# Kernel tuning notes

Measured on AMD Instinct MI355X. Metric: run time of the kernel, lower is better.

## Reference

```python
import jax, jax.numpy as jnp
import numpy as np

B, S, D, H = 2, 2048, 1024, 16
DK = D // H

def setup_inputs() -> dict:
    key = jax.random.key(0)
    ks = jax.random.split(key, 12)
    scale = 1.0 / np.sqrt(D)
    return {
        "q": jax.random.normal(ks[0], (B, S, D), jnp.float32),
        "k": jax.random.normal(ks[1], (B, S, D), jnp.float32),
        "v": jax.random.normal(ks[2], (B, S, D), jnp.float32),
        "mask": jax.random.randint(ks[3], (B, 1, S, S), 0, 2, jnp.int32),
        "w_q": jax.random.normal(ks[4], (D, D), jnp.float32) * scale,
        "b_q": jnp.zeros((D,), jnp.float32),
        "w_k": jax.random.normal(ks[5], (D, D), jnp.float32) * scale,
        "b_k": jnp.zeros((D,), jnp.float32),
        "w_v": jax.random.normal(ks[6], (D, D), jnp.float32) * scale,
        "b_v": jnp.zeros((D,), jnp.float32),
        "w_o": jax.random.normal(ks[7], (D, D), jnp.float32) * scale,
        "b_o": jnp.zeros((D,), jnp.float32),
    }

def reference(q, k, v, mask, w_q, b_q, w_k, b_k, w_v, b_v, w_o, b_o):
    # projections (nn.Linear: x @ W^T + b)
    Q = q @ w_q.T + b_q  # [B,S,D]
    K = k @ w_k.T + b_k
    V = v @ w_v.T + b_v
    # split heads -> [B,H,S,DK]
    Q = Q.reshape(B, S, H, DK).transpose(0, 2, 1, 3)
    K = K.reshape(B, S, H, DK).transpose(0, 2, 1, 3)
    V = V.reshape(B, S, H, DK).transpose(0, 2, 1, 3)
    scores = jnp.einsum("bhqd,bhkd->bhqk", Q, K) / jnp.sqrt(jnp.float32(DK))
    scores = jnp.where(mask == 0, jnp.float32(-1e9), scores)
    attn = jax.nn.softmax(scores, axis=-1)  # dropout p=0 -> identity
    x = jnp.einsum("bhqk,bhkd->bhqd", attn, V)
    x = x.transpose(0, 2, 1, 3).reshape(B, S, D)
    return x @ w_o.T + b_o
```

## Files before the change

### kernel.cpp

```cpp
#include <hip/hip_runtime.h>
#include <hip/hip_bf16.h>
#include <cstdint>
#include <cstddef>

typedef short bf16x8 __attribute__((ext_vector_type(8)));
typedef short bf16x4v __attribute__((ext_vector_type(4)));
typedef float f32x4 __attribute__((ext_vector_type(4)));
typedef __hip_bfloat16 bf16;

constexpr int Bb = 2, Ss = 2048, Dd = 1024, Hh = 16, DKk = 64;

__device__ __forceinline__ void async_lds16(void* lds, const void* g) {
  __builtin_amdgcn_global_load_lds(
      (const __attribute__((address_space(1))) void*)g,
      (__attribute__((address_space(3))) void*)lds, 16, 0, 0);
}

__device__ __forceinline__ float bf2f(bf16 x) { return __bfloat162float(x); }
__device__ __forceinline__ short f2bf(float x) {
  bf16 h = __float2bfloat16(x);
  return *(short*)&h;
}
__device__ __forceinline__ short f2bf_fast(float x) {
  return (short)((__float_as_uint(x) + 0x8000u) >> 16);
}
__device__ __forceinline__ uint32_t pack2bf(float a, float b) {
  return ((__float_as_uint(a) + 0x8000u) >> 16) |
         ((__float_as_uint(b) + 0x8000u) & 0xffff0000u);
}
__device__ __forceinline__ float bfs2f(short s) {
  return __uint_as_float(((uint32_t)(uint16_t)s) << 16);
}

struct CvtArgs {
  const float* src[12];
  short* dst[12];
  int n[12];
  int count;
};

__global__ __launch_bounds__(256)
void cvt_all(CvtArgs a)
{
  const int t = blockIdx.y;
  if (t >= a.count) return;
  const float* s = a.src[t];
  short* d = a.dst[t];
  const int n = a.n[t];
  const int stride = gridDim.x * blockDim.x * 4;
  for (int i = (blockIdx.x * blockDim.x + threadIdx.x) * 4; i < n; i += stride) {
    const float4 v = *(const float4*)(s + i);
    bf16x4v o;
    o[0] = f2bf(v.x); o[1] = f2bf(v.y); o[2] = f2bf(v.z); o[3] = f2bf(v.w);
    *(bf16x4v*)(d + i) = o;
  }
}

__global__ __launch_bounds__(256)
void pack_mask(const int* __restrict__ mask, uint32_t* __restrict__ bits)
{
  const int i = blockIdx.x * 256 + threadIdx.x;
  const unsigned long long bal = __ballot(mask[i] != 0);
  if ((threadIdx.x & 63) == 0)
    *(unsigned long long*)(bits + (i >> 5)) = bal;
}

__global__ __launch_bounds__(256, 3)
void gemm_bt(const bf16* __restrict__ A0, const bf16* __restrict__ A1, const bf16* __restrict__ A2,
             const bf16* __restrict__ W0, const bf16* __restrict__ W1, const bf16* __restrict__ W2,
             const bf16* __restrict__ b0, const bf16* __restrict__ b1, const bf16* __restrict__ b2,
             void* __restrict__ O0, void* __restrict__ O1, void* __restrict__ O2,
             float scale0, int wf32, int vtrans)
{
  extern __shared__ char smem[];
  const int mt  = blockIdx.x;
  const int by  = blockIdx.y;
  const int mat = by >> 3;
  const int nt  = by & 7;
  const bf16* A    = (mat == 0) ? A0 : (mat == 1) ? A1 : A2;
  const bf16* W    = (mat == 0) ? W0 : (mat == 1) ? W1 : W2;
  const bf16* bias = (mat == 0) ? b0 : (mat == 1) ? b1 : b2;
  void*       Out  = (mat == 0) ? O0 : (mat == 1) ? O1 : O2;
  const float scale = (mat == 0) ? scale0 : 1.0f;

  const int tid  = threadIdx.x;
  const int w    = tid >> 6;
  const int lane = tid & 63;
  const int quad = lane >> 4;
  const int l16  = lane & 15;
  const int wm   = (w & 1) * 64;
  const int wn   = (w >> 1) * 64;

  const int srow = lane >> 3;
  const int sseg = (lane & 7) ^ srow;

  const char* Abytes = (const char*)A;
  const char* Wbytes = (const char*)W;

  f32x4 acc[4][4];
#pragma unroll
  for (int i = 0; i < 4; ++i)
#pragma unroll
    for (int j = 0; j < 4; ++j) acc[i][j] = f32x4{0.f, 0.f, 0.f, 0.f};

  for (int kt = 0; kt < 16; ++kt) {
    __syncthreads();
#pragma unroll
    for (int c = 0; c < 4; ++c) {
      const int r0 = w * 32 + c * 8;
      async_lds16(smem + r0 * 128,
                  Abytes + (size_t)(mt * 128 + r0 + srow) * 2048 + kt * 128 + sseg * 16);
      async_lds16(smem + 16384 + r0 * 128,
                  Wbytes + (size_t)(nt * 128 + r0 + srow) * 2048 + kt * 128 + sseg * 16);
    }
    __syncthreads();
#pragma unroll
    for (int s = 0; s < 2; ++s) {
      bf16x8 af[4], bfg[4];
#pragma unroll
      for (int mb = 0; mb < 4; ++mb) {
        const int row = wm + mb * 16 + l16;
        af[mb] = *(const bf16x8*)(smem + row * 128 + (((4 * s + quad) ^ (row & 7)) * 16));
      }
#pragma unroll
      for (int nb = 0; nb < 4; ++nb) {
        const int row = wn + nb * 16 + l16;
        bfg[nb] = *(const bf16x8*)(smem + 16384 + row * 128 + (((4 * s + quad) ^ (row & 7)) * 16));
      }
#pragma unroll
      for (int mb = 0; mb < 4; ++mb)
#pragma unroll
        for (int nb = 0; nb < 4; ++nb)
          acc[mb][nb] = __builtin_amdgcn_mfma_f32_16x16x32_bf16(af[mb], bfg[nb], acc[mb][nb], 0, 0, 0);
    }
  }

  if (vtrans && mat == 2) {
    __syncthreads();
#pragma unroll
    for (int nb = 0; nb < 4; ++nb) {
      const int dk = wn + nb * 16 + l16;
      const float bv = bf2f(bias[nt * 128 + dk]);
#pragma unroll
      for (int mb = 0; mb < 4; ++mb) {
        const int s0 = wm + mb * 16 + quad * 4;
        bf16x4v pk;
#pragma unroll
        for (int r = 0; r < 4; ++r) pk[r] = f2bf_fast(acc[mb][nb][r] + bv);
        *(bf16x4v*)(smem + dk * 256 + (((s0 >> 3) ^ (dk & 15)) * 16) + (s0 & 7) * 2) = pk;
      }
    }
    __syncthreads();
    const int bidx  = (mt * 128) >> 11;
    const int sbase = (mt * 128) & 2047;
#pragma unroll
    for (int i = 0; i < 8; ++i) {
      const int dk  = i * 16 + (tid >> 4);
      const int seg = tid & 15;
      bf16x8 vrow = *(const bf16x8*)(smem + dk * 256 + ((seg ^ (dk & 15)) * 16));
      *(bf16x8*)((bf16*)Out + (size_t)bidx * 2097152 + (size_t)(nt * 128 + dk) * 2048
                 + sbase + seg * 8) = vrow;
    }
  } else {
#pragma unroll
    for (int nb = 0; nb < 4; ++nb) {
      const int col = nt * 128 + wn + nb * 16 + l16;
      const float bv = bf2f(bias[col]);
#pragma unroll
      for (int mb = 0; mb < 4; ++mb) {
#pragma unroll
        for (int r = 0; r < 4; ++r) {
          const int row = mt * 128 + wm + mb * 16 + quad * 4 + r;
          const float val = (acc[mb][nb][r] + bv) * scale;
          const size_t idx = (size_t)row * 1024 + col;
          if (wf32) ((float*)Out)[idx] = val;
          else      ((bf16*)Out)[idx] = *(bf16*)&(short&)*(short[]){f2bf_fast(val)};
        }
      }
    }
  }
}

__global__ __launch_bounds__(256, 3)
void attn(const bf16* __restrict__ Qp, const bf16* __restrict__ Kp,
          const bf16* __restrict__ VpT, const uint32_t* __restrict__ mbits,
          bf16* __restrict__ Opart, float* __restrict__ Lpart)
{
  __shared__ char smem[49152];
  char* Kb = smem;
  char* Vt = smem + 16384;
  char* Ph = smem + 32768;

  const int tile  = blockIdx.x;
  const int split = blockIdx.y;
  const int qt = tile & 15, h = (tile >> 4) & 15, b = tile >> 8;
  const int tid = threadIdx.x, w = tid >> 6, lane = tid & 63;
  const int quad = lane >> 4, l16 = lane & 15;
  const int qb = qt * 128;
  const size_t headoff = (size_t)b * (Ss * Dd) + h * DKk;

  const int kc0 = (split == 0) ? 0 : (split == 1) ? 6 : 11;
  const int kc1 = (split == 0) ? 6 : (split == 1) ? 11 : 16;

  bf16x8 qf[2][2];
#pragma unroll
  for (int set = 0; set < 2; ++set)
#pragma unroll
    for (int s2 = 0; s2 < 2; ++s2) {
      const int row = qb + w * 32 + set * 16 + l16;
      qf[set][s2] = *(const bf16x8*)(Qp + headoff + (size_t)row * Dd + s2 * 32 + quad * 8);
    }

  f32x4 o[2][4];
  float Lacc[2] = {0.f, 0.f};
#pragma unroll
  for (int set = 0; set < 2; ++set)
#pragma unroll
    for (int nbk = 0; nbk < 4; ++nbk) o[set][nbk] = f32x4{0.f, 0.f, 0.f, 0.f};

  const uint32_t* mrow0 = mbits + (size_t)(b * Ss + qb + w * 32 + l16) * 64;
  const uint32_t* mrow1 = mrow0 + 16 * 64;

  char* Preg = (w < 2) ? smem : Ph;
  const int prowbase = (w & 1) * 32;

  for (int kc = kc0; kc < kc1; ++kc) {
    const int kb = kc * 128;
    __syncthreads();
#pragma unroll
    for (int c = 0; c < 4; ++c) {
      {
        const int row = c * 32 + w * 8 + (lane >> 3);
        const int seg = (lane & 7) ^ (row & 7);
        async_lds16(Kb + c * 4096 + w * 1024,
                    Kp + headoff + (size_t)(kb + row) * Dd + seg * 8);
      }
      {
        const int row = c * 16 + w * 4 + (lane >> 4);
        const int seg = (lane & 15) ^ (row & 15);
        async_lds16(Vt + c * 4096 + w * 1024,
                    VpT + (size_t)b * 2097152 + (size_t)(h * 64 + row) * 2048 + kb + seg * 8);
      }
    }
    __syncthreads();

    f32x4 sc[2][8];
#pragma unroll
    for (int set = 0; set < 2; ++set)
#pragma unroll
      for (int nb = 0; nb < 8; ++nb) sc[set][nb] = f32x4{0.f, 0.f, 0.f, 0.f};
#pragma unroll
    for (int s2 = 0; s2 < 2; ++s2)
#pragma unroll
      for (int nb = 0; nb < 8; ++nb) {
        const int row = nb * 16 + l16;
        bf16x8 kf = *(const bf16x8*)(Kb + row * 128 + (((s2 * 4 + quad) ^ (row & 7)) * 16));
        sc[0][nb] = __builtin_amdgcn_mfma_f32_16x16x32_bf16(kf, qf[0][s2], sc[0][nb], 0, 0, 0);
        sc[1][nb] = __builtin_amdgcn_mfma_f32_16x16x32_bf16(kf, qf[1][s2], sc[1][nb], 0, 0, 0);
      }
    __syncthreads();

#pragma unroll
    for (int set = 0; set < 2; ++set) {
      const uint4 mwv = *(const uint4*)((set == 0 ? mrow0 : mrow1) + kc * 4);
      const uint32_t mwa[4] = {mwv.x, mwv.y, mwv.z, mwv.w};
      char* Prow = Preg + (size_t)(prowbase + set * 16 + l16) * 256;
#pragma unroll
      for (int nb = 0; nb < 8; ++nb) {
        const uint32_t nib = (mwa[nb >> 1] >> ((nb & 1) * 16 + quad * 4)) & 0xFu;
        const float p0 = (nib & 1u) ? __expf(sc[set][nb][0]) : 0.f;
        const float p1 = (nib & 2u) ? __expf(sc[set][nb][1]) : 0.f;
        const float p2 = (nib & 4u) ? __expf(sc[set][nb][2]) : 0.f;
        const float p3 = (nib & 8u) ? __expf(sc[set][nb][3]) : 0.f;
        Lacc[set] += (p0 + p1) + (p2 + p3);
        uint2 pk;
        pk.x = pack2bf(p0, p1);
        pk.y = pack2bf(p2, p3);
        *(uint2*)(Prow + (((2 * nb + (quad >> 1)) ^ l16) * 16) + (quad & 1) * 8) = pk;
      }
    }
    asm volatile("s_waitcnt lgkmcnt(0)" ::: "memory");

#pragma unroll
    for (int kb4 = 0; kb4 < 2; ++kb4)
#pragma unroll
      for (int u = 0; u < 2; ++u) {
        bf16x8 pf[2];
#pragma unroll
        for (int set = 0; set < 2; ++set)
          pf[set] = *(const bf16x8*)(Preg + (size_t)(prowbase + set * 16 + l16) * 256 +
                                     (((kb4 * 8 + u * 4 + quad) ^ l16) * 16));
#pragma unroll
        for (int nbk = 0; nbk < 4; ++nbk) {
          const int row = nbk * 16 + l16;
          bf16x8 vf = *(const bf16x8*)(Vt + row * 256 +
                                       (((kb4 * 8 + u * 4 + quad) ^ (row & 15)) * 16));
          o[0][nbk] = __builtin_amdgcn_mfma_f32_16x16x32_bf16(pf[0], vf, o[0][nbk], 0, 0, 0);
          o[1][nbk] = __builtin_amdgcn_mfma_f32_16x16x32_bf16(pf[1], vf, o[1][nbk], 0, 0, 0);
        }
      }
  }

#pragma unroll
  for (int set = 0; set < 2; ++set) {
    float Lq = Lacc[set];
    Lq += __shfl_xor(Lq, 16);
    Lq += __shfl_xor(Lq, 32);
    const int rbase = tile * 128 + w * 32 + set * 16;
#pragma unroll
    for (int r = 0; r < 4; ++r) {
      const int rglob = rbase + quad * 4 + r;
#pragma unroll
      for (int nbk = 0; nbk < 4; ++nbk) {
        short s = f2bf_fast(o[set][nbk][r]);
        ((short*)Opart)[((size_t)split * 65536 + rglob) * 64 + nbk * 16 + l16] = s;
      }
    }
    if (quad == 0)
      Lpart[(size_t)split * 65536 + rbase + l16] = Lq;
  }
}

__global__ __launch_bounds__(256)
void combine(const bf16* __restrict__ Opart, const float* __restrict__ Lpart,
             bf16* __restrict__ Xa)
{
  const int t = threadIdx.x;
  const int row = blockIdx.x * 32 + (t >> 3);
  const int dkc = (t & 7) * 8;
  const float L = Lpart[row] + Lpart[65536 + row] + Lpart[131072 + row];
  const float inv = 1.0f / L;
  const bf16x8 O0 = *(const bf16x8*)(Opart + (size_t)row * 64 + dkc);
  const bf16x8 O1 = *(const bf16x8*)(Opart + ((size_t)65536 + row) * 64 + dkc);
  const bf16x8 O2 = *(const bf16x8*)(Opart + ((size_t)131072 + row) * 64 + dkc);
  bf16x8 res;
#pragma unroll
  for (int j = 0; j < 8; ++j)
    res[j] = f2bf_fast((bfs2f(O0[j]) + bfs2f(O1[j]) + bfs2f(O2[j])) * inv);
  const int tile = row >> 7, qlocal = row & 127;
  const int b = tile >> 8, h = (tile >> 4) & 15, q = (tile & 15) * 128 + qlocal;
  *(bf16x8*)(Xa + (size_t)(b * 2048 + q) * 1024 + h * 64 + dkc) = res;
}

extern "C" void kernel_launch(void* const* d_in, const int* in_sizes, int n_in,
                              void* d_out, int out_size, void* d_ws, size_t ws_size,
                              hipStream_t stream)
{
  const float* q  = (const float*)d_in[0];
  const float* k  = (const float*)d_in[1];
  const float* v  = (const float*)d_in[2];
  const int*   mk = (const int*)d_in[3];
  const float* wq = (const float*)d_in[4];
  const float* bq = (const float*)d_in[5];
  const float* wk = (const float*)d_in[6];
  const float* bk = (const float*)d_in[7];
  const float* wv = (const float*)d_in[8];
  const float* bv = (const float*)d_in[9];
  const float* wo = (const float*)d_in[10];
  const float* bo = (const float*)d_in[11];
  float* out = (float*)d_out;

  char* ws = (char*)d_ws;
  bf16* qb_  = (bf16*)(ws + ((size_t)0  << 20));
  bf16* kb_  = (bf16*)(ws + ((size_t)8  << 20));
  bf16* vb_  = (bf16*)(ws + ((size_t)16 << 20));
  bf16* Qp   = (bf16*)(ws + ((size_t)24 << 20));
  bf16* Kp   = (bf16*)(ws + ((size_t)32 << 20));
  bf16* VpT  = (bf16*)(ws + ((size_t)40 << 20));
  bf16* wqb  = (bf16*)(ws + ((size_t)48 << 20));
  bf16* wkb  = (bf16*)(ws + ((size_t)50 << 20));
  bf16* wvb  = (bf16*)(ws + ((size_t)52 << 20));
  bf16* wob  = (bf16*)(ws + ((size_t)54 << 20));
  bf16* bqb  = (bf16*)(ws + ((size_t)56 << 20));
  bf16* bkb  = (bf16*)(ws + ((size_t)56 << 20) + 2048);
  bf16* bvb  = (bf16*)(ws + ((size_t)56 << 20) + 4096);
  bf16* bob  = (bf16*)(ws + ((size_t)56 << 20) + 6144);
  uint32_t* mbits = (uint32_t*)(ws + ((size_t)56 << 20) + 65536);
  bf16*  Opart = (bf16*)(ws + ((size_t)0 << 20));
  float* Lpart = (float*)(ws + ((size_t)48 << 20));
  bf16*  Xa    = (bf16*)(ws + ((size_t)24 << 20));

  const int NA = Bb * Ss * Dd;
  const int NW = Dd * Dd;

  CvtArgs ca;
  ca.src[0] = q;  ca.dst[0] = (short*)qb_; ca.n[0] = NA;
  ca.src[1] = k;  ca.dst[1] = (short*)kb_; ca.n[1] = NA;
  ca.src[2] = v;  ca.dst[2] = (short*)vb_; ca.n[2] = NA;
  ca.src[3] = wq; ca.dst[3] = (short*)wqb; ca.n[3] = NW;
  ca.src[4] = wk; ca.dst[4] = (short*)wkb; ca.n[4] = NW;
  ca.src[5] = wv; ca.dst[5] = (short*)wvb; ca.n[5] = NW;
  ca.src[6] = wo; ca.dst[6] = (short*)wob; ca.n[6] = NW;
  ca.src[7] = bq; ca.dst[7] = (short*)bqb; ca.n[7] = Dd;
  ca.src[8] = bk; ca.dst[8] = (short*)bkb; ca.n[8] = Dd;
  ca.src[9] = bv; ca.dst[9] = (short*)bvb; ca.n[9] = Dd;
  ca.src[10] = bo; ca.dst[10] = (short*)bob; ca.n[10] = Dd;
  ca.src[11] = bo; ca.dst[11] = (short*)bob; ca.n[11] = 0;
  ca.count = 11;

  dim3 blk(256);
  cvt_all<<<dim3(1024, 11), blk, 0, stream>>>(ca);
  pack_mask<<<dim3(Bb * Ss * Ss / 256), blk, 0, stream>>>(mk, mbits);

  gemm_bt<<<dim3(32, 24), blk, 32768, stream>>>(qb_, kb_, vb_, wqb, wkb, wvb,
                                                bqb, bkb, bvb,
                                                (void*)Qp, (void*)Kp, (void*)VpT,
                                                0.125f, 0, 1);
  attn<<<dim3(512, 3), blk, 0, stream>>>(Qp, Kp, VpT, mbits, Opart, Lpart);
  combine<<<dim3(2048), blk, 0, stream>>>(Opart, Lpart, Xa);
  gemm_bt<<<dim3(32, 8), blk, 32768, stream>>>(Xa, Xa, Xa, wob, wob, wob,
                                               bob, bob, bob,
                                               (void*)out, (void*)out, (void*)out,
                                               1.0f, 1, 0);
}
```

Baseline: 281.5 us.

## Fuse mask packing into conversion kernel and add smaller-tile output GEMM

Mask bit-packing moves into the conversion kernel as an extra grid row, which removes one kernel launch. The output projection gets its own kernel with 64x64 tiles, giving 1024 blocks instead of 256 with 128x128 tiles, so more of the GPU's compute units are kept busy. The general GEMM loses its fp32-write branch. The new output kernel has no double buffering and a lower MFMA-per-load ratio, which may cost memory efficiency.

```diff
diff --git a/kernel.cpp b/kernel.cpp
--- a/kernel.cpp
+++ b/kernel.cpp
@@ -40,9 +40,20 @@
 };
 
 __global__ __launch_bounds__(256)
-void cvt_all(CvtArgs a)
+void cvt_all(CvtArgs a, const int* __restrict__ mask, uint32_t* __restrict__ bits)
 {
   const int t = blockIdx.y;
+  if (t == 11) {
+    const int stride = 1024 * 256;
+    int i = blockIdx.x * 256 + threadIdx.x;
+#pragma unroll 4
+    for (int it = 0; it < 32; ++it, i += stride) {
+      const unsigned long long bal = __ballot(mask[i] != 0);
+      if ((threadIdx.x & 63) == 0)
+        *(unsigned long long*)(bits + (i >> 5)) = bal;
+    }
+    return;
+  }
   if (t >= a.count) return;
   const float* s = a.src[t];
   short* d = a.dst[t];
@@ -56,21 +67,12 @@
   }
 }
 
-__global__ __launch_bounds__(256)
-void pack_mask(const int* __restrict__ mask, uint32_t* __restrict__ bits)
-{
-  const int i = blockIdx.x * 256 + threadIdx.x;
-  const unsigned long long bal = __ballot(mask[i] != 0);
-  if ((threadIdx.x & 63) == 0)
-    *(unsigned long long*)(bits + (i >> 5)) = bal;
-}
-
 __global__ __launch_bounds__(256, 3)
 void gemm_bt(const bf16* __restrict__ A0, const bf16* __restrict__ A1, const bf16* __restrict__ A2,
              const bf16* __restrict__ W0, const bf16* __restrict__ W1, const bf16* __restrict__ W2,
              const bf16* __restrict__ b0, const bf16* __restrict__ b1, const bf16* __restrict__ b2,
              void* __restrict__ O0, void* __restrict__ O1, void* __restrict__ O2,
-             float scale0, int wf32, int vtrans)
+             float scale0, int vtrans)
 {
   extern __shared__ char smem[];
   const int mt  = blockIdx.x;
@@ -171,11 +173,78 @@
 #pragma unroll
         for (int r = 0; r < 4; ++r) {
           const int row = mt * 128 + wm + mb * 16 + quad * 4 + r;
-          const float val = (acc[mb][nb][r] + bv) * scale;
-          const size_t idx = (size_t)row * 1024 + col;
-          if (wf32) ((float*)Out)[idx] = val;
-          else      ((bf16*)Out)[idx] = *(bf16*)&(short&)*(short[]){f2bf_fast(val)};
+          short s = f2bf_fast((acc[mb][nb][r] + bv) * scale);
+          ((short*)Out)[(size_t)row * 1024 + col] = s;
         }
+      }
+    }
+  }
+}
+
+__global__ __launch_bounds__(256, 4)
+void gemm_out(const bf16* __restrict__ A, const bf16* __restrict__ W,
+              const bf16* __restrict__ bias, float* __restrict__ Out)
+{
+  __shared__ char smem[16384];
+  const int mt = blockIdx.x;
+  const int nt = blockIdx.y;
+  const int tid = threadIdx.x, w = tid >> 6, lane = tid & 63;
+  const int quad = lane >> 4, l16 = lane & 15;
+  const int wm = (w & 1) * 32, wn = (w >> 1) * 32;
+  const int srow = lane >> 3;
+  const int sseg = (lane & 7) ^ (srow & 7);
+
+  const char* Abytes = (const char*)A;
+  const char* Wbytes = (const char*)W;
+
+  f32x4 acc[2][2];
+#pragma unroll
+  for (int i = 0; i < 2; ++i)
+#pragma unroll
+    for (int j = 0; j < 2; ++j) acc[i][j] = f32x4{0.f, 0.f, 0.f, 0.f};
+
+  for (int kt = 0; kt < 16; ++kt) {
+    __syncthreads();
+#pragma unroll
+    for (int c = 0; c < 2; ++c) {
+      const int r0 = c * 32 + w * 8;
+      async_lds16(smem + c * 4096 + w * 1024,
+                  Abytes + (size_t)(mt * 64 + r0 + srow) * 2048 + kt * 128 + sseg * 16);
+      async_lds16(smem + 8192 + c * 4096 + w * 1024,
+                  Wbytes + (size_t)(nt * 64 + r0 + srow) * 2048 + kt * 128 + sseg * 16);
+    }
+    __syncthreads();
+#pragma unroll
+    for (int s = 0; s < 2; ++s) {
+      bf16x8 af[2], bfg[2];
+#pragma unroll
+      for (int mb = 0; mb < 2; ++mb) {
+        const int row = wm + mb * 16 + l16;
+        af[mb] = *(const bf16x8*)(smem + row * 128 + (((4 * s + quad) ^ (row & 7)) * 16));
+      }
+#pragma unroll
+      for (int nb = 0; nb < 2; ++nb) {
+        const int row = wn + nb * 16 + l16;
+        bfg[nb] = *(const bf16x8*)(smem + 8192 + row * 128 + (((4 * s + quad) ^ (row & 7)) * 16));
+      }
+#pragma unroll
+      for (int mb = 0; mb < 2; ++mb)
+#pragma unroll
+        for (int nb = 0; nb < 2; ++nb)
+          acc[mb][nb] = __builtin_amdgcn_mfma_f32_16x16x32_bf16(af[mb], bfg[nb], acc[mb][nb], 0, 0, 0);
+    }
+  }
+
+#pragma unroll
+  for (int nb = 0; nb < 2; ++nb) {
+    const int col = nt * 64 + wn + nb * 16 + l16;
+    const float bv = bf2f(bias[col]);
+#pragma unroll
+    for (int mb = 0; mb < 2; ++mb) {
+#pragma unroll
+      for (int r = 0; r < 4; ++r) {
+        const int row = mt * 64 + wm + mb * 16 + quad * 4 + r;
+        Out[(size_t)row * 1024 + col] = acc[mb][nb][r] + bv;
       }
     }
   }
@@ -399,17 +468,13 @@
   ca.count = 11;
 
   dim3 blk(256);
-  cvt_all<<<dim3(1024, 11), blk, 0, stream>>>(ca);
-  pack_mask<<<dim3(Bb * Ss * Ss / 256), blk, 0, stream>>>(mk, mbits);
+  cvt_all<<<dim3(1024, 12), blk, 0, stream>>>(ca, mk, mbits);
 
   gemm_bt<<<dim3(32, 24), blk, 32768, stream>>>(qb_, kb_, vb_, wqb, wkb, wvb,
                                                 bqb, bkb, bvb,
                                                 (void*)Qp, (void*)Kp, (void*)VpT,
-                                                0.125f, 0, 1);
+                                                0.125f, 1);
   attn<<<dim3(512, 3), blk, 0, stream>>>(Qp, Kp, VpT, mbits, Opart, Lpart);
   combine<<<dim3(2048), blk, 0, stream>>>(Opart, Lpart, Xa);
-  gemm_bt<<<dim3(32, 8), blk, 32768, stream>>>(Xa, Xa, Xa, wob, wob, wob,
-                                               bob, bob, bob,
-                                               (void*)out, (void*)out, (void*)out,
-                                               1.0f, 1, 0);
-}
+  gemm_out<<<dim3(64, 16), blk, 0, stream>>>(Xa, wob, bob, out);
+}
```

After: 280.2 us. Within noise of the previous version (-0.5%).
